# Kernel optimization log

Measured on AMD Instinct MI355X. Metric: run time of the kernel, lower is better.

## Reference

```python
import jax, jax.numpy as jnp
import numpy as np

N, B, D, A, E, H = 8, 32768, 128, 64, 32, 128


def setup_inputs() -> dict:
    key = jax.random.key(0)
    ks = jax.random.split(key, 22)
    g = lambda k, shape: (jax.random.normal(k, shape, dtype=jnp.float32) * 0.1)
    return {
        "states": jax.random.normal(ks[0], (N, B, D), dtype=jnp.float32),
        # per-agent DQN (2-hidden-layer MLP), stacked over agents
        "W1": g(ks[1], (N, D, H)), "b1": g(ks[2], (N, H)),
        "W2": g(ks[3], (N, H, H)), "b2": g(ks[4], (N, H)),
        "W3": g(ks[5], (N, H, A)), "b3": g(ks[6], (N, A)),
        # per-agent query MLP
        "Wq1": g(ks[7], (N, D, E)), "bq1": g(ks[8], (N, E)),
        "Wq2": g(ks[9], (N, E, E)), "bq2": g(ks[10], (N, E)),
        # per-agent key Linear
        "Wk": g(ks[11], (N, D, E)), "bk": g(ks[12], (N, E)),
        # shared scaling MLP (D->1->1)
        "Ws1": g(ks[13], (D, 1)), "bs1": g(ks[14], (1,)),
        "Ws2": g(ks[15], (1, 1)), "bs2": g(ks[16], (1,)),
        # shared constraint MLP (D->E->1)
        "Wc1": g(ks[17], (D, E)), "bc1": g(ks[18], (E,)),
        "Wc2": g(ks[19], (E, 1)), "bc2": g(ks[20], (1,)),
    }


def reference(states, W1, b1, W2, b2, W3, b3, Wq1, bq1, Wq2, bq2, Wk, bk,
              Ws1, bs1, Ws2, bs2, Wc1, bc1, Wc2, bc2):
    relu = jax.nn.relu
    # per-agent DQN -> q_values [B, N, A]
    h = relu(jnp.einsum('nbd,ndh->nbh', states, W1) + b1[:, None, :])
    h = relu(jnp.einsum('nbh,nhk->nbk', h, W2) + b2[:, None, :])
    q_values = (jnp.einsum('nbh,nha->nba', h, W3) + b3[:, None, :]).transpose(1, 0, 2)
    # per-agent keys [B, N, E]
    keys = (jnp.einsum('nbd,nde->nbe', states, Wk) + bk[:, None, :]).transpose(1, 0, 2)
    # per-agent queries [B, N, E]
    qh = relu(jnp.einsum('nbd,nde->nbe', states, Wq1) + bq1[:, None, :])
    queries = (jnp.einsum('nbe,nef->nbf', qh, Wq2) + bq2[:, None, :]).transpose(1, 0, 2)
    # attention [B, N, N]
    scores = jnp.einsum('bnd,bmd->bnm', queries, keys) / jnp.sqrt(jnp.float32(E))
    attn = jax.nn.softmax(scores, axis=-1)
    # faithful to original einsum 'bnm,bna->bna' (sums attn over m)
    weighted_qs = jnp.einsum('bnm,bna->bna', attn, q_values)
    # shared scaling MLP, sigmoid gate [B, N, 1]
    s = relu(jnp.einsum('nbd,do->nbo', states, Ws1) + bs1)
    s = jnp.einsum('nbo,op->nbp', s, Ws2) + bs2
    scaling = jax.nn.sigmoid(s.transpose(1, 0, 2))
    summed_q = jnp.mean(scaling * weighted_qs, axis=1)  # [B, A]
    # shared constraint MLP [B, N, 1] -> mean over agents [B, 1]
    c = relu(jnp.einsum('nbd,de->nbe', states, Wc1) + bc1)
    c = (jnp.einsum('nbe,eo->nbo', c, Wc2) + bc2).transpose(1, 0, 2)
    c = jnp.mean(c, axis=1)
    return summed_q + c  # [B, A]
```

## Files before the change

kernel.cpp:

```cpp
#include <hip/hip_runtime.h>
#include <hip/hip_bf16.h>

#define NAG 8
#define BATCH 32768
#define DDIM 128
#define ADIM 64
#define HDIM 128

#define NJ1 11
#define NJ2 8
#define NJ3 4
#define FB_L1 (NJ1*4)
#define FB_L2 (NJ2*4)
#define FB_L3 (NJ3*4)
#define FB_B  (FB_L2+FB_L3)
#define FB_TOT (FB_L1+FB_L2+FB_L3)
#define WAGENT (FB_TOT*512)

typedef __attribute__((ext_vector_type(8))) short bf16x8;
typedef __attribute__((ext_vector_type(4))) float f32x4;
typedef __attribute__((ext_vector_type(4))) unsigned int u32x4;

static __device__ __forceinline__ unsigned short f2bf(float f) {
  unsigned int u = __builtin_bit_cast(unsigned int, f);
  u += 0x7fffu + ((u >> 16) & 1u);
  return (unsigned short)(u >> 16);
}

static __device__ __forceinline__ unsigned int cvt_pk_bf16(float a, float b) {
  unsigned int r;
  asm("v_cvt_pk_bf16_f32 %0, %1, %2" : "=v"(r) : "v"(a), "v"(b));
  return r;
}

static __device__ __forceinline__ void gload_lds16(const void* g, void* l) {
  __builtin_amdgcn_global_load_lds(
      (const __attribute__((address_space(1))) unsigned int*)g,
      (__attribute__((address_space(3))) unsigned int*)l, 16, 0, 0);
}

__global__ void __launch_bounds__(256)
prep_weights(const float* __restrict__ W1, const float* __restrict__ W2,
             const float* __restrict__ W3, const float* __restrict__ Wc1,
             const float* __restrict__ Ws1, const float* __restrict__ b1,
             const float* __restrict__ bc1, const float* __restrict__ bs1,
             unsigned short* __restrict__ wbuf, float* __restrict__ b1e)
{
  int tid = blockIdx.x * 256 + threadIdx.x;
  if (tid < NAG * WAGENT) {
    int agent = tid / WAGENT;
    int rem   = tid % WAGENT;
    int fb = rem >> 9;
    int li = rem & 511;
    int l = li >> 3, t = li & 7;
    int lr = l & 15, lg = l >> 4;
    float v = 0.0f;
    if (fb < FB_L1) {
      int j = fb >> 2, kk = fb & 3;
      int col = j*16 + lr, k = kk*32 + lg*8 + t;
      if (col < 128)       v = W1[((size_t)agent*128 + k)*128 + col];
      else if (col < 160)  v = Wc1[k*32 + (col-128)];
      else if (col == 160) v = Ws1[k];
    } else if (fb < FB_L1 + FB_L2) {
      int f = fb - FB_L1;
      int j = f >> 2, kk = f & 3;
      int col = j*16 + lr, k = kk*32 + lg*8 + t;
      v = W2[((size_t)agent*128 + k)*128 + col];
    } else {
      int f = fb - FB_L1 - FB_L2;
      int j = f >> 2, kk = f & 3;
      int col = j*16 + lr, k = kk*32 + lg*8 + t;
      v = W3[((size_t)agent*128 + k)*64 + col];
    }
    wbuf[tid] = f2bf(v);
  }
  if (tid < NAG * 176) {
    int agent = tid / 176, col = tid % 176;
    float v = 0.0f;
    if (col < 128)       v = b1[agent*128 + col];
    else if (col < 160)  v = bc1[col - 128];
    else if (col == 160) v = bs1[0];
    b1e[tid] = v;
  }
}

__global__ void __launch_bounds__(512, 1)
qatten_main(const float* __restrict__ states,
            const float* __restrict__ b2g, const float* __restrict__ b3g,
            const float* __restrict__ ws2p, const float* __restrict__ bs2p,
            const float* __restrict__ wc2g, const float* __restrict__ bc2p,
            const unsigned short* __restrict__ wbuf,
            const float* __restrict__ b1e,
            float* __restrict__ out)
{
  __shared__ __align__(16) unsigned short bufA[FB_L1*512];
  __shared__ __align__(16) unsigned short bufB[FB_B*512];
  __shared__ __align__(16) unsigned short hlds[8 * 2048];

  const int tid  = threadIdx.x;
  const int wave = tid >> 6;
  const int lane = tid & 63;
  const int lr   = lane & 15;
  const int lg   = lane >> 4;
  const int row0 = blockIdx.x * 128 + wave * 16;

  unsigned short* hp = hlds + wave * 2048;

  const float ws2  = ws2p[0];
  const float bs2v = bs2p[0];
  const float bc2v = bc2p[0];
  const float wc2a = wc2g[lr];
  const float wc2b = wc2g[16 + lr];

  const f32x4 zero4 = {0.f, 0.f, 0.f, 0.f};

  f32x4 out_acc[NJ3];
#pragma unroll
  for (int j = 0; j < NJ3; ++j) out_acc[j] = zero4;

  {
    const char* sA = (const char*)wbuf;
    for (int c = wave; c < FB_L1; c += 8)
      gload_lds16(sA + c*1024 + lane*16, (char*)bufA + c*1024);
    const char* sB = (const char*)(wbuf + FB_L1*512);
    for (int c = wave; c < FB_B; c += 8)
      gload_lds16(sB + c*1024 + lane*16, (char*)bufB + c*1024);
  }
  __syncthreads();

  for (int a = 0; a < NAG; ++a) {
    float b1v[NJ1], b2v[NJ2], b3v[NJ3];
#pragma unroll
    for (int j = 0; j < NJ1; ++j) b1v[j] = b1e[a*176 + j*16 + lr];
#pragma unroll
    for (int j = 0; j < NJ2; ++j) b2v[j] = b2g[a*HDIM + j*16 + lr];
#pragma unroll
    for (int j = 0; j < NJ3; ++j) b3v[j] = b3g[a*ADIM + j*16 + lr];

    bf16x8 afr[4];
    {
      const float* sb = states + ((size_t)a * BATCH + row0) * DDIM;
#pragma unroll
      for (int kk = 0; kk < 4; ++kk) {
        const float* p = sb + lr*DDIM + kk*32 + lg*8;
        f32x4 v0 = *(const f32x4*)p;
        f32x4 v1 = *(const f32x4*)(p + 4);
        u32x4 w;
        w[0] = cvt_pk_bf16(v0[0], v0[1]);
        w[1] = cvt_pk_bf16(v0[2], v0[3]);
        w[2] = cvt_pk_bf16(v1[0], v1[1]);
        w[3] = cvt_pk_bf16(v1[2], v1[3]);
        afr[kk] = __builtin_bit_cast(bf16x8, w);
      }
    }

    f32x4 eacc[3];
    {
      bf16x8 pf[2][4];
#pragma unroll
      for (int kk = 0; kk < 4; ++kk)
        pf[0][kk] = *(const bf16x8*)&bufA[kk*512 + lane*8];
#pragma unroll
      for (int j = 0; j < 11; ++j) {
        if (j < 10) {
#pragma unroll
          for (int kk = 0; kk < 4; ++kk)
            pf[(j+1)&1][kk] = *(const bf16x8*)&bufA[((j+1)*4 + kk)*512 + lane*8];
        }
        f32x4 acc = zero4;
#pragma unroll
        for (int kk = 0; kk < 4; ++kk)
          acc = __builtin_amdgcn_mfma_f32_16x16x32_bf16(afr[kk], pf[j&1][kk], acc, 0, 0, 0);
        if (j < 8) {
#pragma unroll
          for (int r = 0; r < 4; ++r) {
            float hv = acc[r] + b1v[j];
            hv = hv > 0.f ? hv : 0.f;
            int row = lg*4 + r;
            int bo = row*256 + (((j*16 + lr)*2) ^ ((row & 7) << 4));
            *(unsigned short*)((char*)hp + bo) = f2bf(hv);
          }
        } else {
          eacc[j-8] = acc;
        }
      }
    }

    float scl[4], crow[4];
#pragma unroll
    for (int r = 0; r < 4; ++r) {
      float c0 = eacc[0][r] + b1v[8];  c0 = c0 > 0.f ? c0 : 0.f;
      float c1 = eacc[1][r] + b1v[9];  c1 = c1 > 0.f ? c1 : 0.f;
      float cd = c0*wc2a + c1*wc2b;
      cd += __shfl_xor(cd, 1);
      cd += __shfl_xor(cd, 2);
      cd += __shfl_xor(cd, 4);
      cd += __shfl_xor(cd, 8);
      crow[r] = cd + bc2v;
      float sp = eacc[2][r] + b1v[10];
      sp = __shfl(sp, lane & 48);
      sp = sp > 0.f ? sp : 0.f;
      float s = ws2 * sp + bs2v;
      scl[r] = 1.f / (1.f + __expf(-s));
    }

    __syncthreads();

    if (a < NAG-1) {
      const char* sA = (const char*)(wbuf + (size_t)(a+1)*WAGENT);
      for (int c = wave; c < FB_L1; c += 8)
        gload_lds16(sA + c*1024 + lane*16, (char*)bufA + c*1024);
    }

#pragma unroll
    for (int kk = 0; kk < 4; ++kk) {
      int row = lr;
      int bo = row*256 + ((kk*64 + lg*16) ^ ((row & 7) << 4));
      afr[kk] = *(const bf16x8*)((char*)hp + bo);
    }

    {
      bf16x8 pf[2][4];
#pragma unroll
      for (int kk = 0; kk < 4; ++kk)
        pf[0][kk] = *(const bf16x8*)&bufB[kk*512 + lane*8];
#pragma unroll
      for (int j = 0; j < 8; ++j) {
        if (j < 7) {
#pragma unroll
          for (int kk = 0; kk < 4; ++kk)
            pf[(j+1)&1][kk] = *(const bf16x8*)&bufB[((j+1)*4 + kk)*512 + lane*8];
        }
        f32x4 acc = zero4;
#pragma unroll
        for (int kk = 0; kk < 4; ++kk)
          acc = __builtin_amdgcn_mfma_f32_16x16x32_bf16(afr[kk], pf[j&1][kk], acc, 0, 0, 0);
#pragma unroll
        for (int r = 0; r < 4; ++r) {
          float hv = acc[r] + b2v[j];
          hv = hv > 0.f ? hv : 0.f;
          int row = lg*4 + r;
          int bo = row*256 + (((j*16 + lr)*2) ^ ((row & 7) << 4));
          *(unsigned short*)((char*)hp + bo) = f2bf(hv);
        }
      }
    }

#pragma unroll
    for (int kk = 0; kk < 4; ++kk) {
      int row = lr;
      int bo = row*256 + ((kk*64 + lg*16) ^ ((row & 7) << 4));
      afr[kk] = *(const bf16x8*)((char*)hp + bo);
    }

    {
      bf16x8 pf[2][4];
#pragma unroll
      for (int kk = 0; kk < 4; ++kk)
        pf[0][kk] = *(const bf16x8*)&bufB[(FB_L2 + kk)*512 + lane*8];
#pragma unroll
      for (int j = 0; j < NJ3; ++j) {
        if (j < NJ3-1) {
#pragma unroll
          for (int kk = 0; kk < 4; ++kk)
            pf[(j+1)&1][kk] = *(const bf16x8*)&bufB[(FB_L2 + (j+1)*4 + kk)*512 + lane*8];
        }
        f32x4 acc = zero4;
#pragma unroll
        for (int kk = 0; kk < 4; ++kk)
          acc = __builtin_amdgcn_mfma_f32_16x16x32_bf16(afr[kk], pf[j&1][kk], acc, 0, 0, 0);
#pragma unroll
        for (int r = 0; r < 4; ++r)
          out_acc[j][r] += scl[r] * (acc[r] + b3v[j]) + crow[r];
      }
    }

    __syncthreads();

    if (a < NAG-1) {
      const char* sB = (const char*)(wbuf + (size_t)(a+1)*WAGENT + FB_L1*512);
      for (int c = wave; c < FB_B; c += 8)
        gload_lds16(sB + c*1024 + lane*16, (char*)bufB + c*1024);
    }
  }

#pragma unroll
  for (int j = 0; j < NJ3; ++j)
#pragma unroll
    for (int r = 0; r < 4; ++r) {
      size_t row = (size_t)row0 + lg*4 + r;
      out[row*ADIM + j*16 + lr] = out_acc[j][r] * 0.125f;
    }
}

extern "C" void kernel_launch(void* const* d_in, const int* in_sizes, int n_in,
                              void* d_out, int out_size, void* d_ws, size_t ws_size,
                              hipStream_t stream)
{
  const float* states = (const float*)d_in[0];
  const float* W1  = (const float*)d_in[1];
  const float* b1  = (const float*)d_in[2];
  const float* W2  = (const float*)d_in[3];
  const float* b2  = (const float*)d_in[4];
  const float* W3  = (const float*)d_in[5];
  const float* b3  = (const float*)d_in[6];
  const float* Ws1 = (const float*)d_in[13];
  const float* bs1 = (const float*)d_in[14];
  const float* Ws2 = (const float*)d_in[15];
  const float* bs2 = (const float*)d_in[16];
  const float* Wc1 = (const float*)d_in[17];
  const float* bc1 = (const float*)d_in[18];
  const float* Wc2 = (const float*)d_in[19];
  const float* bc2 = (const float*)d_in[20];

  unsigned short* wbuf = (unsigned short*)d_ws;
  float* b1e = (float*)((char*)d_ws + (size_t)NAG * WAGENT * 2);

  dim3 pb(256), pg((NAG * WAGENT + 255) / 256);
  prep_weights<<<pg, pb, 0, stream>>>(W1, W2, W3, Wc1, Ws1, b1, bc1, bs1, wbuf, b1e);

  dim3 mb(512), mg(BATCH / 128);
  qatten_main<<<mg, mb, 0, stream>>>(states, b2, b3, Ws2, bs2, Wc2, bc2,
                                     wbuf, b1e, (float*)d_out);
}
```

Measured before the change: 65.36 us.

## Prefetch next agent's states and biases into registers, deepen LDS weight prefetch

Loads the next agent's state rows and bias values into registers while the current agent's MLP runs, which hides global memory latency across the agent loop. Deepens the LDS weight-fragment prefetch from double to triple buffering. Moves the hidden-activation read for layer 2 to before the barrier. The extra live registers (8 f32x4 states, 23 biases, a third fragment buffer) may raise register pressure and lower occupancy.

```diff
diff --git a/kernel.cpp b/kernel.cpp
--- a/kernel.cpp
+++ b/kernel.cpp
@@ -126,51 +126,82 @@
     for (int c = wave; c < FB_B; c += 8)
       gload_lds16(sB + c*1024 + lane*16, (char*)bufB + c*1024);
   }
+
+  f32x4 sreg[8];
+  float b1n[NJ1], b2n[NJ2], b3n[NJ3];
+  {
+    const float* sb = states + (size_t)row0 * DDIM;
+#pragma unroll
+    for (int kk = 0; kk < 4; ++kk) {
+      const float* p = sb + lr*DDIM + kk*32 + lg*8;
+      sreg[kk*2]   = *(const f32x4*)p;
+      sreg[kk*2+1] = *(const f32x4*)(p + 4);
+    }
+#pragma unroll
+    for (int j = 0; j < NJ1; ++j) b1n[j] = b1e[j*16 + lr];
+#pragma unroll
+    for (int j = 0; j < NJ2; ++j) b2n[j] = b2g[j*16 + lr];
+#pragma unroll
+    for (int j = 0; j < NJ3; ++j) b3n[j] = b3g[j*16 + lr];
+  }
   __syncthreads();
 
   for (int a = 0; a < NAG; ++a) {
     float b1v[NJ1], b2v[NJ2], b3v[NJ3];
 #pragma unroll
-    for (int j = 0; j < NJ1; ++j) b1v[j] = b1e[a*176 + j*16 + lr];
-#pragma unroll
-    for (int j = 0; j < NJ2; ++j) b2v[j] = b2g[a*HDIM + j*16 + lr];
-#pragma unroll
-    for (int j = 0; j < NJ3; ++j) b3v[j] = b3g[a*ADIM + j*16 + lr];
+    for (int j = 0; j < NJ1; ++j) b1v[j] = b1n[j];
+#pragma unroll
+    for (int j = 0; j < NJ2; ++j) b2v[j] = b2n[j];
+#pragma unroll
+    for (int j = 0; j < NJ3; ++j) b3v[j] = b3n[j];
 
     bf16x8 afr[4];
-    {
-      const float* sb = states + ((size_t)a * BATCH + row0) * DDIM;
+#pragma unroll
+    for (int kk = 0; kk < 4; ++kk) {
+      f32x4 v0 = sreg[kk*2], v1 = sreg[kk*2+1];
+      u32x4 w;
+      w[0] = cvt_pk_bf16(v0[0], v0[1]);
+      w[1] = cvt_pk_bf16(v0[2], v0[3]);
+      w[2] = cvt_pk_bf16(v1[0], v1[1]);
+      w[3] = cvt_pk_bf16(v1[2], v1[3]);
+      afr[kk] = __builtin_bit_cast(bf16x8, w);
+    }
+
+    if (a < NAG-1) {
+      const float* sb = states + ((size_t)(a+1) * BATCH + row0) * DDIM;
 #pragma unroll
       for (int kk = 0; kk < 4; ++kk) {
         const float* p = sb + lr*DDIM + kk*32 + lg*8;
-        f32x4 v0 = *(const f32x4*)p;
-        f32x4 v1 = *(const f32x4*)(p + 4);
-        u32x4 w;
-        w[0] = cvt_pk_bf16(v0[0], v0[1]);
-        w[1] = cvt_pk_bf16(v0[2], v0[3]);
-        w[2] = cvt_pk_bf16(v1[0], v1[1]);
-        w[3] = cvt_pk_bf16(v1[2], v1[3]);
-        afr[kk] = __builtin_bit_cast(bf16x8, w);
-      }
+        sreg[kk*2]   = *(const f32x4*)p;
+        sreg[kk*2+1] = *(const f32x4*)(p + 4);
+      }
+#pragma unroll
+      for (int j = 0; j < NJ1; ++j) b1n[j] = b1e[(a+1)*176 + j*16 + lr];
+#pragma unroll
+      for (int j = 0; j < NJ2; ++j) b2n[j] = b2g[(a+1)*HDIM + j*16 + lr];
+#pragma unroll
+      for (int j = 0; j < NJ3; ++j) b3n[j] = b3g[(a+1)*ADIM + j*16 + lr];
     }
 
     f32x4 eacc[3];
     {
-      bf16x8 pf[2][4];
-#pragma unroll
-      for (int kk = 0; kk < 4; ++kk)
-        pf[0][kk] = *(const bf16x8*)&bufA[kk*512 + lane*8];
+      bf16x8 pf[3][4];
+#pragma unroll
+      for (int kk = 0; kk < 4; ++kk) {
+        pf[0][kk] = *(const bf16x8*)&bufA[(0*4 + kk)*512 + lane*8];
+        pf[1][kk] = *(const bf16x8*)&bufA[(1*4 + kk)*512 + lane*8];
+      }
 #pragma unroll
       for (int j = 0; j < 11; ++j) {
-        if (j < 10) {
+        if (j + 2 <= 10) {
 #pragma unroll
           for (int kk = 0; kk < 4; ++kk)
-            pf[(j+1)&1][kk] = *(const bf16x8*)&bufA[((j+1)*4 + kk)*512 + lane*8];
+            pf[(j+2)%3][kk] = *(const bf16x8*)&bufA[((j+2)*4 + kk)*512 + lane*8];
         }
         f32x4 acc = zero4;
 #pragma unroll
         for (int kk = 0; kk < 4; ++kk)
-          acc = __builtin_amdgcn_mfma_f32_16x16x32_bf16(afr[kk], pf[j&1][kk], acc, 0, 0, 0);
+          acc = __builtin_amdgcn_mfma_f32_16x16x32_bf16(afr[kk], pf[j%3][kk], acc, 0, 0, 0);
         if (j < 8) {
 #pragma unroll
           for (int r = 0; r < 4; ++r) {
@@ -204,6 +235,13 @@
       scl[r] = 1.f / (1.f + __expf(-s));
     }
 
+#pragma unroll
+    for (int kk = 0; kk < 4; ++kk) {
+      int row = lr;
+      int bo = row*256 + ((kk*64 + lg*16) ^ ((row & 7) << 4));
+      afr[kk] = *(const bf16x8*)((char*)hp + bo);
+    }
+
     __syncthreads();
 
     if (a < NAG-1) {
@@ -212,29 +250,24 @@
         gload_lds16(sA + c*1024 + lane*16, (char*)bufA + c*1024);
     }
 
-#pragma unroll
-    for (int kk = 0; kk < 4; ++kk) {
-      int row = lr;
-      int bo = row*256 + ((kk*64 + lg*16) ^ ((row & 7) << 4));
-      afr[kk] = *(const bf16x8*)((char*)hp + bo);
-    }
-
     {
-      bf16x8 pf[2][4];
-#pragma unroll
-      for (int kk = 0; kk < 4; ++kk)
-        pf[0][kk] = *(const bf16x8*)&bufB[kk*512 + lane*8];
+      bf16x8 pf[3][4];
+#pragma unroll
+      for (int kk = 0; kk < 4; ++kk) {
+        pf[0][kk] = *(const bf16x8*)&bufB[(0*4 + kk)*512 + lane*8];
+        pf[1][kk] = *(const bf16x8*)&bufB[(1*4 + kk)*512 + lane*8];
+      }
 #pragma unroll
       for (int j = 0; j < 8; ++j) {
-        if (j < 7) {
+        if (j + 2 <= 7) {
 #pragma unroll
           for (int kk = 0; kk < 4; ++kk)
-            pf[(j+1)&1][kk] = *(const bf16x8*)&bufB[((j+1)*4 + kk)*512 + lane*8];
+            pf[(j+2)%3][kk] = *(const bf16x8*)&bufB[((j+2)*4 + kk)*512 + lane*8];
         }
         f32x4 acc = zero4;
 #pragma unroll
         for (int kk = 0; kk < 4; ++kk)
-          acc = __builtin_amdgcn_mfma_f32_16x16x32_bf16(afr[kk], pf[j&1][kk], acc, 0, 0, 0);
+          acc = __builtin_amdgcn_mfma_f32_16x16x32_bf16(afr[kk], pf[j%3][kk], acc, 0, 0, 0);
 #pragma unroll
         for (int r = 0; r < 4; ++r) {
           float hv = acc[r] + b2v[j];
```

Result: faster. 62.93 us (-3.7%).

## Split agents across grid.y, double rows per wave, prefetch states into registers

Applied to the files above, without the earlier changes.

Each wave now handles 32 rows (two 16-row MFMA tiles) so every LDS weight fragment is reused across two row tiles. Agents are split into two halves along grid.y, and the partial sums are combined with atomicAdd into an output that is zeroed by a memset. The next agent's states are prefetched into registers during the current agent's compute. The cost is higher register pressure, double the LDS for hidden activations, atomic traffic, and an extra memset launch.

```diff
diff --git a/kernel.cpp b/kernel.cpp
--- a/kernel.cpp
+++ b/kernel.cpp
@@ -95,16 +95,17 @@
 {
   __shared__ __align__(16) unsigned short bufA[FB_L1*512];
   __shared__ __align__(16) unsigned short bufB[FB_B*512];
-  __shared__ __align__(16) unsigned short hlds[8 * 2048];
+  __shared__ __align__(16) unsigned short hlds[8 * 4096];
 
   const int tid  = threadIdx.x;
   const int wave = tid >> 6;
   const int lane = tid & 63;
   const int lr   = lane & 15;
   const int lg   = lane >> 4;
-  const int row0 = blockIdx.x * 128 + wave * 16;
-
-  unsigned short* hp = hlds + wave * 2048;
+  const int row0 = blockIdx.x * 256 + wave * 32;
+  const int abase = blockIdx.y * 4;
+
+  unsigned short* hp = hlds + wave * 4096;
 
   const float ws2  = ws2p[0];
   const float bs2v = bs2p[0];
@@ -114,21 +115,38 @@
 
   const f32x4 zero4 = {0.f, 0.f, 0.f, 0.f};
 
-  f32x4 out_acc[NJ3];
-#pragma unroll
-  for (int j = 0; j < NJ3; ++j) out_acc[j] = zero4;
+  f32x4 out_acc[2][NJ3];
+#pragma unroll
+  for (int m = 0; m < 2; ++m)
+#pragma unroll
+    for (int j = 0; j < NJ3; ++j) out_acc[m][j] = zero4;
 
   {
-    const char* sA = (const char*)wbuf;
+    const char* sA = (const char*)(wbuf + (size_t)abase * WAGENT);
     for (int c = wave; c < FB_L1; c += 8)
       gload_lds16(sA + c*1024 + lane*16, (char*)bufA + c*1024);
-    const char* sB = (const char*)(wbuf + FB_L1*512);
+    const char* sB = sA + FB_L1*1024;
     for (int c = wave; c < FB_B; c += 8)
       gload_lds16(sB + c*1024 + lane*16, (char*)bufB + c*1024);
   }
+
+  f32x4 sreg[16];
+  {
+    const float* sb = states + ((size_t)abase * BATCH + row0) * DDIM;
+#pragma unroll
+    for (int m = 0; m < 2; ++m)
+#pragma unroll
+      for (int kk = 0; kk < 4; ++kk) {
+        const float* p = sb + (m*16 + lr)*DDIM + kk*32 + lg*8;
+        sreg[m*8 + kk*2]     = *(const f32x4*)p;
+        sreg[m*8 + kk*2 + 1] = *(const f32x4*)(p + 4);
+      }
+  }
   __syncthreads();
 
-  for (int a = 0; a < NAG; ++a) {
+  for (int a4 = 0; a4 < 4; ++a4) {
+    const int a = abase + a4;
+
     float b1v[NJ1], b2v[NJ2], b3v[NJ3];
 #pragma unroll
     for (int j = 0; j < NJ1; ++j) b1v[j] = b1e[a*176 + j*16 + lr];
@@ -137,24 +155,33 @@
 #pragma unroll
     for (int j = 0; j < NJ3; ++j) b3v[j] = b3g[a*ADIM + j*16 + lr];
 
-    bf16x8 afr[4];
-    {
-      const float* sb = states + ((size_t)a * BATCH + row0) * DDIM;
+    bf16x8 afr[2][4];
+#pragma unroll
+    for (int m = 0; m < 2; ++m)
 #pragma unroll
       for (int kk = 0; kk < 4; ++kk) {
-        const float* p = sb + lr*DDIM + kk*32 + lg*8;
-        f32x4 v0 = *(const f32x4*)p;
-        f32x4 v1 = *(const f32x4*)(p + 4);
+        f32x4 v0 = sreg[m*8 + kk*2], v1 = sreg[m*8 + kk*2 + 1];
         u32x4 w;
         w[0] = cvt_pk_bf16(v0[0], v0[1]);
         w[1] = cvt_pk_bf16(v0[2], v0[3]);
         w[2] = cvt_pk_bf16(v1[0], v1[1]);
         w[3] = cvt_pk_bf16(v1[2], v1[3]);
-        afr[kk] = __builtin_bit_cast(bf16x8, w);
-      }
-    }
-
-    f32x4 eacc[3];
+        afr[m][kk] = __builtin_bit_cast(bf16x8, w);
+      }
+
+    if (a4 < 3) {
+      const float* sb = states + ((size_t)(a+1) * BATCH + row0) * DDIM;
+#pragma unroll
+      for (int m = 0; m < 2; ++m)
+#pragma unroll
+        for (int kk = 0; kk < 4; ++kk) {
+          const float* p = sb + (m*16 + lr)*DDIM + kk*32 + lg*8;
+          sreg[m*8 + kk*2]     = *(const f32x4*)p;
+          sreg[m*8 + kk*2 + 1] = *(const f32x4*)(p + 4);
+        }
+    }
+
+    f32x4 eacc[3][2];
     {
       bf16x8 pf[2][4];
 #pragma unroll
@@ -167,96 +194,108 @@
           for (int kk = 0; kk < 4; ++kk)
             pf[(j+1)&1][kk] = *(const bf16x8*)&bufA[((j+1)*4 + kk)*512 + lane*8];
         }
-        f32x4 acc = zero4;
-#pragma unroll
-        for (int kk = 0; kk < 4; ++kk)
-          acc = __builtin_amdgcn_mfma_f32_16x16x32_bf16(afr[kk], pf[j&1][kk], acc, 0, 0, 0);
-        if (j < 8) {
+#pragma unroll
+        for (int m = 0; m < 2; ++m) {
+          f32x4 acc = zero4;
+#pragma unroll
+          for (int kk = 0; kk < 4; ++kk)
+            acc = __builtin_amdgcn_mfma_f32_16x16x32_bf16(afr[m][kk], pf[j&1][kk], acc, 0, 0, 0);
+          if (j < 8) {
+#pragma unroll
+            for (int r = 0; r < 4; ++r) {
+              float hv = acc[r] + b1v[j];
+              hv = hv > 0.f ? hv : 0.f;
+              int row = m*16 + lg*4 + r;
+              int bo = row*256 + (((j*16 + lr)*2) ^ ((row & 7) << 4));
+              *(unsigned short*)((char*)hp + bo) = f2bf(hv);
+            }
+          } else {
+            eacc[j-8][m] = acc;
+          }
+        }
+      }
+    }
+
+    float scl[2][4], crow[2][4];
+#pragma unroll
+    for (int m = 0; m < 2; ++m)
+#pragma unroll
+      for (int r = 0; r < 4; ++r) {
+        float c0 = eacc[0][m][r] + b1v[8];  c0 = c0 > 0.f ? c0 : 0.f;
+        float c1 = eacc[1][m][r] + b1v[9];  c1 = c1 > 0.f ? c1 : 0.f;
+        float cd = c0*wc2a + c1*wc2b;
+        cd += __shfl_xor(cd, 1);
+        cd += __shfl_xor(cd, 2);
+        cd += __shfl_xor(cd, 4);
+        cd += __shfl_xor(cd, 8);
+        crow[m][r] = cd + bc2v;
+        float sp = eacc[2][m][r] + b1v[10];
+        sp = __shfl(sp, lane & 48);
+        sp = sp > 0.f ? sp : 0.f;
+        float s = ws2 * sp + bs2v;
+        scl[m][r] = 1.f / (1.f + __expf(-s));
+      }
+
+#pragma unroll
+    for (int m = 0; m < 2; ++m)
+#pragma unroll
+      for (int kk = 0; kk < 4; ++kk) {
+        int row = m*16 + lr;
+        int bo = row*256 + ((kk*64 + lg*16) ^ ((row & 7) << 4));
+        afr[m][kk] = *(const bf16x8*)((char*)hp + bo);
+      }
+
+    __syncthreads();
+
+    if (a4 < 3) {
+      const char* sA = (const char*)(wbuf + (size_t)(a+1)*WAGENT);
+      for (int c = wave; c < FB_L1; c += 8)
+        gload_lds16(sA + c*1024 + lane*16, (char*)bufA + c*1024);
+    }
+
+    {
+      bf16x8 pf[2][4];
+#pragma unroll
+      for (int kk = 0; kk < 4; ++kk)
+        pf[0][kk] = *(const bf16x8*)&bufB[kk*512 + lane*8];
+#pragma unroll
+      for (int j = 0; j < 8; ++j) {
+        if (j < 7) {
+#pragma unroll
+          for (int kk = 0; kk < 4; ++kk)
+            pf[(j+1)&1][kk] = *(const bf16x8*)&bufB[((j+1)*4 + kk)*512 + lane*8];
+        }
+#pragma unroll
+        for (int m = 0; m < 2; ++m) {
+          f32x4 acc = zero4;
+#pragma unroll
+          for (int kk = 0; kk < 4; ++kk)
+            acc = __builtin_amdgcn_mfma_f32_16x16x32_bf16(afr[m][kk], pf[j&1][kk], acc, 0, 0, 0);
 #pragma unroll
           for (int r = 0; r < 4; ++r) {
-            float hv = acc[r] + b1v[j];
+            float hv = acc[r] + b2v[j];
             hv = hv > 0.f ? hv : 0.f;
-            int row = lg*4 + r;
+            int row = m*16 + lg*4 + r;
             int bo = row*256 + (((j*16 + lr)*2) ^ ((row & 7) << 4));
             *(unsigned short*)((char*)hp + bo) = f2bf(hv);
           }
-        } else {
-          eacc[j-8] = acc;
-        }
-      }
-    }
-
-    float scl[4], crow[4];
-#pragma unroll
-    for (int r = 0; r < 4; ++r) {
-      float c0 = eacc[0][r] + b1v[8];  c0 = c0 > 0.f ? c0 : 0.f;
-      float c1 = eacc[1][r] + b1v[9];  c1 = c1 > 0.f ? c1 : 0.f;
-      float cd = c0*wc2a + c1*wc2b;
-      cd += __shfl_xor(cd, 1);
-      cd += __shfl_xor(cd, 2);
-      cd += __shfl_xor(cd, 4);
-      cd += __shfl_xor(cd, 8);
-      crow[r] = cd + bc2v;
-      float sp = eacc[2][r] + b1v[10];
-      sp = __shfl(sp, lane & 48);
-      sp = sp > 0.f ? sp : 0.f;
-      float s = ws2 * sp + bs2v;
-      scl[r] = 1.f / (1.f + __expf(-s));
-    }
-
-    __syncthreads();
-
-    if (a < NAG-1) {
-      const char* sA = (const char*)(wbuf + (size_t)(a+1)*WAGENT);
-      for (int c = wave; c < FB_L1; c += 8)
-        gload_lds16(sA + c*1024 + lane*16, (char*)bufA + c*1024);
-    }
-
-#pragma unroll
-    for (int kk = 0; kk < 4; ++kk) {
-      int row = lr;
-      int bo = row*256 + ((kk*64 + lg*16) ^ ((row & 7) << 4));
-      afr[kk] = *(const bf16x8*)((char*)hp + bo);
-    }
+        }
+      }
+    }
+
+#pragma unroll
+    for (int m = 0; m < 2; ++m)
+#pragma unroll
+      for (int kk = 0; kk < 4; ++kk) {
+        int row = m*16 + lr;
+        int bo = row*256 + ((kk*64 + lg*16) ^ ((row & 7) << 4));
+        afr[m][kk] = *(const bf16x8*)((char*)hp + bo);
+      }
 
     {
       bf16x8 pf[2][4];
 #pragma unroll
       for (int kk = 0; kk < 4; ++kk)
-        pf[0][kk] = *(const bf16x8*)&bufB[kk*512 + lane*8];
-#pragma unroll
-      for (int j = 0; j < 8; ++j) {
-        if (j < 7) {
-#pragma unroll
-          for (int kk = 0; kk < 4; ++kk)
-            pf[(j+1)&1][kk] = *(const bf16x8*)&bufB[((j+1)*4 + kk)*512 + lane*8];
-        }
-        f32x4 acc = zero4;
-#pragma unroll
-        for (int kk = 0; kk < 4; ++kk)
-          acc = __builtin_amdgcn_mfma_f32_16x16x32_bf16(afr[kk], pf[j&1][kk], acc, 0, 0, 0);
-#pragma unroll
-        for (int r = 0; r < 4; ++r) {
-          float hv = acc[r] + b2v[j];
-          hv = hv > 0.f ? hv : 0.f;
-          int row = lg*4 + r;
-          int bo = row*256 + (((j*16 + lr)*2) ^ ((row & 7) << 4));
-          *(unsigned short*)((char*)hp + bo) = f2bf(hv);
-        }
-      }
-    }
-
-#pragma unroll
-    for (int kk = 0; kk < 4; ++kk) {
-      int row = lr;
-      int bo = row*256 + ((kk*64 + lg*16) ^ ((row & 7) << 4));
-      afr[kk] = *(const bf16x8*)((char*)hp + bo);
-    }
-
-    {
-      bf16x8 pf[2][4];
-#pragma unroll
-      for (int kk = 0; kk < 4; ++kk)
         pf[0][kk] = *(const bf16x8*)&bufB[(FB_L2 + kk)*512 + lane*8];
 #pragma unroll
       for (int j = 0; j < NJ3; ++j) {
@@ -265,19 +304,22 @@
           for (int kk = 0; kk < 4; ++kk)
             pf[(j+1)&1][kk] = *(const bf16x8*)&bufB[(FB_L2 + (j+1)*4 + kk)*512 + lane*8];
         }
-        f32x4 acc = zero4;
-#pragma unroll
-        for (int kk = 0; kk < 4; ++kk)
-          acc = __builtin_amdgcn_mfma_f32_16x16x32_bf16(afr[kk], pf[j&1][kk], acc, 0, 0, 0);
-#pragma unroll
-        for (int r = 0; r < 4; ++r)
-          out_acc[j][r] += scl[r] * (acc[r] + b3v[j]) + crow[r];
+#pragma unroll
+        for (int m = 0; m < 2; ++m) {
+          f32x4 acc = zero4;
+#pragma unroll
+          for (int kk = 0; kk < 4; ++kk)
+            acc = __builtin_amdgcn_mfma_f32_16x16x32_bf16(afr[m][kk], pf[j&1][kk], acc, 0, 0, 0);
+#pragma unroll
+          for (int r = 0; r < 4; ++r)
+            out_acc[m][j][r] += scl[m][r] * (acc[r] + b3v[j]) + crow[m][r];
+        }
       }
     }
 
     __syncthreads();
 
-    if (a < NAG-1) {
+    if (a4 < 3) {
       const char* sB = (const char*)(wbuf + (size_t)(a+1)*WAGENT + FB_L1*512);
       for (int c = wave; c < FB_B; c += 8)
         gload_lds16(sB + c*1024 + lane*16, (char*)bufB + c*1024);
@@ -285,12 +327,14 @@
   }
 
 #pragma unroll
-  for (int j = 0; j < NJ3; ++j)
-#pragma unroll
-    for (int r = 0; r < 4; ++r) {
-      size_t row = (size_t)row0 + lg*4 + r;
-      out[row*ADIM + j*16 + lr] = out_acc[j][r] * 0.125f;
-    }
+  for (int m = 0; m < 2; ++m)
+#pragma unroll
+    for (int j = 0; j < NJ3; ++j)
+#pragma unroll
+      for (int r = 0; r < 4; ++r) {
+        size_t row = (size_t)row0 + m*16 + lg*4 + r;
+        atomicAdd(&out[row*ADIM + j*16 + lr], out_acc[m][j][r] * 0.125f);
+      }
 }
 
 extern "C" void kernel_launch(void* const* d_in, const int* in_sizes, int n_in,
@@ -316,10 +360,12 @@
   unsigned short* wbuf = (unsigned short*)d_ws;
   float* b1e = (float*)((char*)d_ws + (size_t)NAG * WAGENT * 2);
 
+  hipMemsetAsync(d_out, 0, (size_t)out_size * sizeof(float), stream);
+
   dim3 pb(256), pg((NAG * WAGENT + 255) / 256);
   prep_weights<<<pg, pb, 0, stream>>>(W1, W2, W3, Wc1, Ws1, b1, bc1, bs1, wbuf, b1e);
 
-  dim3 mb(512), mg(BATCH / 128);
+  dim3 mb(512), mg(BATCH / 256, 2);
   qatten_main<<<mg, mb, 0, stream>>>(states, b2, b3, Ws2, bs2, Wc2, bc2,
                                      wbuf, b1e, (float*)d_out);
 }
```

Measured after the change: 94.87 us. 1.45x slower.
